# Kernel tuning notes

Measured on AMD Instinct MI355X. Metric: run time of the kernel, lower is better.

## Reference

```python
import jax, jax.numpy as jnp
import numpy as np

N_NODES = 50000
N_EDGES = 800000
IN_DIM, HIDDEN, Z_DIM = 32, 64, 32


def gcn_conv(x, W, b, src, dst, n):
    """PyG-style GCNConv: h = D^{-1/2}(A+I)D^{-1/2} (x W) + b."""
    h = x @ W  # [N, out]
    loop = jnp.arange(n, dtype=src.dtype)
    s = jnp.concatenate([src, loop])  # add self-loops
    d = jnp.concatenate([dst, loop])
    deg = jax.ops.segment_sum(jnp.ones(s.shape, h.dtype), d, num_segments=n)
    dinv = jax.lax.rsqrt(jnp.maximum(deg, jnp.asarray(1.0, h.dtype)))
    norm = dinv[s] * dinv[d]                       # [E+N]
    msg = h[s] * norm[:, None]                     # gather + scale
    out = jax.ops.segment_sum(msg, d, num_segments=n)  # scatter-add
    return out + b


def setup_inputs() -> dict:
    key = jax.random.key(0)
    ks = jax.random.split(key, 8)
    sc = lambda fan_in: 1.0 / np.sqrt(fan_in)
    x = jax.random.normal(ks[0], (N_NODES, IN_DIM), jnp.float32)
    edge_index = jax.random.randint(ks[1], (2, N_EDGES), 0, N_NODES, jnp.int64)
    W1 = jax.random.normal(ks[2], (IN_DIM, HIDDEN), jnp.float32) * sc(IN_DIM)
    b1 = jnp.zeros((HIDDEN,), jnp.float32)
    W2 = jax.random.normal(ks[3], (HIDDEN, HIDDEN), jnp.float32) * sc(HIDDEN)
    b2 = jnp.zeros((HIDDEN,), jnp.float32)
    W_mu = jax.random.normal(ks[4], (HIDDEN, Z_DIM), jnp.float32) * sc(HIDDEN)
    b_mu = jnp.zeros((Z_DIM,), jnp.float32)
    W_lv = jax.random.normal(ks[5], (HIDDEN, Z_DIM), jnp.float32) * sc(HIDDEN)
    b_lv = jnp.zeros((Z_DIM,), jnp.float32)
    eps = jax.random.normal(ks[6], (N_NODES, Z_DIM), jnp.float32)
    return {"x": x, "edge_index": edge_index, "W1": W1, "b1": b1, "W2": W2,
            "b2": b2, "W_mu": W_mu, "b_mu": b_mu, "W_lv": W_lv, "b_lv": b_lv,
            "eps": eps}


def reference(x, edge_index, W1, b1, W2, b2, W_mu, b_mu, W_lv, b_lv, eps):
    src, dst = edge_index[0], edge_index[1]
    n = x.shape[0]
    h = jax.nn.relu(gcn_conv(x, W1, b1, src, dst, n))
    h = jax.nn.relu(gcn_conv(h, W2, b2, src, dst, n))
    # dropout p=0.0 -> identity
    mu = gcn_conv(h, W_mu, b_mu, src, dst, n)
    logvar = gcn_conv(h, W_lv, b_lv, src, dst, n)
    z = mu + jnp.exp(0.5 * logvar) * eps  # reparametrize
    return (z, mu, logvar)
```

## Files before the change

### kernel.cpp

```cpp
#include <hip/hip_runtime.h>
#include <math.h>

#define N_NODES 50000
#define N_EDGES 800000
#define IN_DIM 32
#define HIDDEN 64
#define Z_DIM 32
#define SCAN_B 256
#define NB_SCAN ((N_NODES + SCAN_B - 1) / SCAN_B)
#define N_XCD 8
#define NPX ((N_NODES + N_XCD - 1) / N_XCD)
#define SLICE 2048
#define N_SLICE ((N_EDGES + SLICE - 1) / SLICE)
#define SCAT_B (N_SLICE * N_XCD)
#define FB 2048

__device__ __forceinline__ float bf2f(unsigned short u) {
    return __uint_as_float(((unsigned int)u) << 16);
}
__device__ __forceinline__ unsigned short f2bf(float f) {
    unsigned int u = __float_as_uint(f);
    u += 0x7fffu + ((u >> 16) & 1u);
    return (unsigned short)(u >> 16);
}

__device__ __forceinline__ int detect64(const int* raw) {
    int lane = threadIdx.x & 63;
    int odd = raw[2 * lane + 1];
    unsigned long long b = __ballot(odd != 0);
    return (b == 0ULL) ? 1 : 0;
}

__global__ void prep_kernel(const float* __restrict__ x, unsigned short* __restrict__ xb,
                            const void* __restrict__ raw, int* __restrict__ flag,
                            int* __restrict__ cnt, int2* __restrict__ ep0,
                            int* __restrict__ rank) {
    int is64 = detect64((const int*)raw);
    int i = blockIdx.x * 256 + threadIdx.x;
    if (blockIdx.x == 0 && threadIdx.x == 0) *flag = is64;
    if (i < N_NODES * IN_DIM) xb[i] = f2bf(x[i]);
    if (blockIdx.x < SCAT_B) {
        int xcd = blockIdx.x % N_XCD;
        int sl  = blockIdx.x / N_XCD;
        int own = ((sl % N_XCD) == xcd) ? 1 : 0;
        int lo  = xcd * NPX, hi = lo + NPX;
        int base = sl * SLICE;
#pragma unroll
        for (int j = 0; j < SLICE / 256; j++) {
            int e = base + j * 256 + threadIdx.x;
            if (e < N_EDGES) {
                int d = is64 ? (int)((const long long*)raw)[N_EDGES + e]
                             : ((const int*)raw)[N_EDGES + e];
                if (own) {
                    int s = is64 ? (int)((const long long*)raw)[e]
                                 : ((const int*)raw)[e];
                    ep0[e] = make_int2(s, d);
                }
                if (d >= lo && d < hi) rank[e] = atomicAdd(&cnt[d], 1);
            }
        }
    }
}

__global__ void scan1_kernel(const int* __restrict__ cnt, int* __restrict__ pre,
                             int* __restrict__ bsum, float* __restrict__ dinv) {
    __shared__ int s[SCAN_B];
    int t = threadIdx.x;
    int g = blockIdx.x * SCAN_B + t;
    int v = (g < N_NODES) ? cnt[g] : 0;
    if (g < N_NODES) dinv[g] = rsqrtf((float)(v + 1));
    s[t] = v;
    __syncthreads();
    for (int o = 1; o < SCAN_B; o <<= 1) {
        int add = (t >= o) ? s[t - o] : 0;
        __syncthreads();
        s[t] += add;
        __syncthreads();
    }
    if (g < N_NODES) pre[g] = s[t] - v;
    if (t == SCAN_B - 1) bsum[blockIdx.x] = s[t];
}

__global__ void scan23_kernel(int* __restrict__ rowptr, const int* __restrict__ bsum) {
    __shared__ int s[256];
    int t = threadIdx.x;
    int v = (t < NB_SCAN) ? bsum[t] : 0;
    s[t] = v;
    __syncthreads();
    for (int o = 1; o < 256; o <<= 1) {
        int add = (t >= o) ? s[t - o] : 0;
        __syncthreads();
        s[t] += add;
        __syncthreads();
    }
    int excl = s[blockIdx.x] - bsum[blockIdx.x];
    int g = blockIdx.x * SCAN_B + t;
    if (g < N_NODES) rowptr[g] += excl;
    if (g == 0) rowptr[N_NODES] = N_EDGES;
}

__global__ __launch_bounds__(256) void scatter_kernel(
        const int2* __restrict__ ep0, const int* __restrict__ rank,
        const int* __restrict__ rowptr, const float* __restrict__ dinv,
        int2* __restrict__ ep) {
    int base = blockIdx.x * SLICE;
#pragma unroll
    for (int j = 0; j < SLICE / 256; j++) {
        int e = base + j * 256 + threadIdx.x;
        if (e < N_EDGES) {
            int2 sd = ep0[e];
            int p = rowptr[sd.y] + rank[e];
            ep[p] = make_int2(sd.x, __float_as_int(dinv[sd.x]));
        }
    }
}

__device__ __forceinline__ void agg_body64(int e0, int e1, int2 pr,
                                           const int2* __restrict__ ep,
                                           const uint2* __restrict__ g2,
                                           int lane, float acc[4]) {
    int gsel = lane >> 4;
    int c    = lane & 15;
    for (int base = e0; base < e1; base += 64) {
        int cnt = e1 - base; cnt = cnt > 64 ? 64 : cnt;
        for (int j = 0; j < cnt; j += 16) {
            uint2 fv[4]; float wv[4];
#pragma unroll
            for (int u = 0; u < 4; u++) {
                int idx = j + u * 4 + gsel;
                int cl  = idx < cnt ? idx : cnt - 1;
                int s   = __builtin_amdgcn_ds_bpermute(cl << 2, pr.x);
                int w   = __builtin_amdgcn_ds_bpermute(cl << 2, pr.y);
                wv[u]   = idx < cnt ? __int_as_float(w) : 0.0f;
                fv[u]   = g2[(size_t)s * 16 + c];
            }
#pragma unroll
            for (int u = 0; u < 4; u++) {
                acc[0] = fmaf(wv[u], __uint_as_float(fv[u].x << 16),         acc[0]);
                acc[1] = fmaf(wv[u], __uint_as_float(fv[u].x & 0xffff0000u), acc[1]);
                acc[2] = fmaf(wv[u], __uint_as_float(fv[u].y << 16),         acc[2]);
                acc[3] = fmaf(wv[u], __uint_as_float(fv[u].y & 0xffff0000u), acc[3]);
            }
        }
        int nb = base + 64;
        if (nb < e1) {
            int idx = nb + lane;
            pr = ep[idx < N_EDGES ? idx : (N_EDGES - 1)];
        }
    }
}

__device__ __forceinline__ void agg_body32(int e0, int e1, int2 pr,
                                           const int2* __restrict__ ep,
                                           const uint2* __restrict__ x2,
                                           int lane, float acc[4]) {
    int gsel = lane >> 3;
    int c    = lane & 7;
    for (int base = e0; base < e1; base += 64) {
        int cnt = e1 - base; cnt = cnt > 64 ? 64 : cnt;
        for (int j = 0; j < cnt; j += 16) {
            uint2 fv[2]; float wv[2];
#pragma unroll
            for (int u = 0; u < 2; u++) {
                int idx = j + u * 8 + gsel;
                int cl  = idx < cnt ? idx : cnt - 1;
                int s   = __builtin_amdgcn_ds_bpermute(cl << 2, pr.x);
                int w   = __builtin_amdgcn_ds_bpermute(cl << 2, pr.y);
                wv[u]   = idx < cnt ? __int_as_float(w) : 0.0f;
                fv[u]   = x2[(size_t)s * 8 + c];
            }
#pragma unroll
            for (int u = 0; u < 2; u++) {
                acc[0] = fmaf(wv[u], __uint_as_float(fv[u].x << 16),         acc[0]);
                acc[1] = fmaf(wv[u], __uint_as_float(fv[u].x & 0xffff0000u), acc[1]);
                acc[2] = fmaf(wv[u], __uint_as_float(fv[u].y << 16),         acc[2]);
                acc[3] = fmaf(wv[u], __uint_as_float(fv[u].y & 0xffff0000u), acc[3]);
            }
        }
        int nb = base + 64;
        if (nb < e1) {
            int idx = nb + lane;
            pr = ep[idx < N_EDGES ? idx : (N_EDGES - 1)];
        }
    }
}

__global__ __launch_bounds__(256, 4) void fused_layer32_kernel(
        const int* __restrict__ rowptr, const int2* __restrict__ ep,
        const float* __restrict__ dinv, const unsigned short* __restrict__ xb,
        const float* __restrict__ W1, const float* __restrict__ b1,
        unsigned short* __restrict__ out) {
    __shared__ float sq[4 * 32];
    int lane = threadIdx.x & 63;
    int wav  = threadIdx.x >> 6;
    int gsel = lane >> 3;
    int c    = lane & 7;
    const uint2* x2 = (const uint2*)xb;
    float wcol[IN_DIM];
#pragma unroll
    for (int k = 0; k < IN_DIM; k++) wcol[k] = W1[k * 64 + lane];
    float bb = b1[lane];
    int wid = __builtin_amdgcn_readfirstlane((int)((blockIdx.x * blockDim.x + threadIdx.x) >> 6));
    int nw  = (gridDim.x * blockDim.x) >> 6;
    int v = wid;
    if (v >= N_NODES) return;
    int e0 = rowptr[v], e1 = rowptr[v + 1];
    float dv = dinv[v];
    uint2 hv = x2[(size_t)v * 8 + c];
    int i0 = e0 + lane;
    int2 pr = ep[i0 < N_EDGES ? i0 : (N_EDGES - 1)];
    while (v < N_NODES) {
        int vn = v + nw;
        int e0n = 0, e1n = 0;
        float dvn = 0.0f;
        uint2 hvn = make_uint2(0, 0);
        int2 prn = make_int2(0, 0);
        if (vn < N_NODES) {
            e0n = rowptr[vn]; e1n = rowptr[vn + 1];
            dvn = dinv[vn];
            hvn = x2[(size_t)vn * 8 + c];
            int in0 = e0n + lane;
            prn = ep[in0 < N_EDGES ? in0 : (N_EDGES - 1)];
        }
        float sv = (gsel == 0) ? dv : 0.0f;
        float acc[4];
        acc[0] = sv * __uint_as_float(hv.x << 16);
        acc[1] = sv * __uint_as_float(hv.x & 0xffff0000u);
        acc[2] = sv * __uint_as_float(hv.y << 16);
        acc[3] = sv * __uint_as_float(hv.y & 0xffff0000u);
        agg_body32(e0, e1, pr, ep, x2, lane, acc);
#pragma unroll
        for (int i = 0; i < 4; i++) {
            acc[i] += __shfl_xor(acc[i], 8);
            acc[i] += __shfl_xor(acc[i], 16);
            acc[i] += __shfl_xor(acc[i], 32);
        }
        if (lane < 8)
            ((float4*)(sq + wav * 32))[c] =
                make_float4(dv * acc[0], dv * acc[1], dv * acc[2], dv * acc[3]);
        float o = bb;
        const float4* q4 = (const float4*)(sq + wav * 32);
#pragma unroll
        for (int k = 0; k < IN_DIM / 4; k++) {
            float4 t = q4[k];
            o = fmaf(t.x, wcol[4 * k + 0], o);
            o = fmaf(t.y, wcol[4 * k + 1], o);
            o = fmaf(t.z, wcol[4 * k + 2], o);
            o = fmaf(t.w, wcol[4 * k + 3], o);
        }
        out[(size_t)v * 64 + lane] = f2bf(fmaxf(o, 0.0f));
        v = vn; e0 = e0n; e1 = e1n; dv = dvn; hv = hvn; pr = prn;
    }
}

__global__ __launch_bounds__(256, 4) void fused_layer64_kernel(
        const int* __restrict__ rowptr, const int2* __restrict__ ep,
        const float* __restrict__ dinv, const unsigned short* __restrict__ g,
        const float* __restrict__ W, const float* __restrict__ bias,
        unsigned short* __restrict__ out) {
    __shared__ float sq[4 * 64];
    int lane = threadIdx.x & 63;
    int wav  = threadIdx.x >> 6;
    int gsel = lane >> 4;
    int c    = lane & 15;
    const uint2* g2 = (const uint2*)g;
    float wcol[HIDDEN];
#pragma unroll
    for (int k = 0; k < HIDDEN; k++) wcol[k] = W[k * 64 + lane];
    float bb = bias[lane];
    int wid = __builtin_amdgcn_readfirstlane((int)((blockIdx.x * blockDim.x + threadIdx.x) >> 6));
    int nw  = (gridDim.x * blockDim.x) >> 6;
    int v = wid;
    if (v >= N_NODES) return;
    int e0 = rowptr[v], e1 = rowptr[v + 1];
    float dv = dinv[v];
    uint2 hv = g2[(size_t)v * 16 + c];
    int i0 = e0 + lane;
    int2 pr = ep[i0 < N_EDGES ? i0 : (N_EDGES - 1)];
    while (v < N_NODES) {
        int vn = v + nw;
        int e0n = 0, e1n = 0;
        float dvn = 0.0f;
        uint2 hvn = make_uint2(0, 0);
        int2 prn = make_int2(0, 0);
        if (vn < N_NODES) {
            e0n = rowptr[vn]; e1n = rowptr[vn + 1];
            dvn = dinv[vn];
            hvn = g2[(size_t)vn * 16 + c];
            int in0 = e0n + lane;
            prn = ep[in0 < N_EDGES ? in0 : (N_EDGES - 1)];
        }
        float sv = (gsel == 0) ? dv : 0.0f;
        float acc[4];
        acc[0] = sv * __uint_as_float(hv.x << 16);
        acc[1] = sv * __uint_as_float(hv.x & 0xffff0000u);
        acc[2] = sv * __uint_as_float(hv.y << 16);
        acc[3] = sv * __uint_as_float(hv.y & 0xffff0000u);
        agg_body64(e0, e1, pr, ep, g2, lane, acc);
#pragma unroll
        for (int i = 0; i < 4; i++) {
            acc[i] += __shfl_xor(acc[i], 16);
            acc[i] += __shfl_xor(acc[i], 32);
        }
        if (lane < 16)
            ((float4*)(sq + wav * 64))[c] =
                make_float4(dv * acc[0], dv * acc[1], dv * acc[2], dv * acc[3]);
        float o = bb;
        const float4* q4 = (const float4*)(sq + wav * 64);
#pragma unroll
        for (int k = 0; k < HIDDEN / 4; k++) {
            float4 t = q4[k];
            o = fmaf(t.x, wcol[4 * k + 0], o);
            o = fmaf(t.y, wcol[4 * k + 1], o);
            o = fmaf(t.z, wcol[4 * k + 2], o);
            o = fmaf(t.w, wcol[4 * k + 3], o);
        }
        out[(size_t)v * 64 + lane] = f2bf(fmaxf(o, 0.0f));
        v = vn; e0 = e0n; e1 = e1n; dv = dvn; hv = hvn; pr = prn;
    }
}

__global__ __launch_bounds__(256, 4) void fused_head_kernel(
        const int* __restrict__ rowptr, const int2* __restrict__ ep,
        const float* __restrict__ dinv, const unsigned short* __restrict__ g,
        const float* __restrict__ Wmu, const float* __restrict__ Wlv,
        const float* __restrict__ bmu, const float* __restrict__ blv,
        const float* __restrict__ eps, float* __restrict__ outz) {
    __shared__ float sq[4 * 64];
    int lane = threadIdx.x & 63;
    int wav  = threadIdx.x >> 6;
    int gsel = lane >> 4;
    int c    = lane & 15;
    int f = lane & 31;
    bool hi = lane >= 32;
    const uint2* g2 = (const uint2*)g;
    float wcol[HIDDEN];
#pragma unroll
    for (int k = 0; k < HIDDEN; k++)
        wcol[k] = hi ? Wlv[k * 32 + f] : Wmu[k * 32 + f];
    float bb = hi ? blv[f] : bmu[f];
    float* z  = outz;
    float* mu = outz + (size_t)N_NODES * Z_DIM;
    float* lv = outz + 2 * (size_t)N_NODES * Z_DIM;
    int wid = __builtin_amdgcn_readfirstlane((int)((blockIdx.x * blockDim.x + threadIdx.x) >> 6));
    int nw  = (gridDim.x * blockDim.x) >> 6;
    int v = wid;
    if (v >= N_NODES) return;
    int e0 = rowptr[v], e1 = rowptr[v + 1];
    float dv = dinv[v];
    uint2 hv = g2[(size_t)v * 16 + c];
    int i0 = e0 + lane;
    int2 pr = ep[i0 < N_EDGES ? i0 : (N_EDGES - 1)];
    while (v < N_NODES) {
        int vn = v + nw;
        int e0n = 0, e1n = 0;
        float dvn = 0.0f;
        uint2 hvn = make_uint2(0, 0);
        int2 prn = make_int2(0, 0);
        if (vn < N_NODES) {
            e0n = rowptr[vn]; e1n = rowptr[vn + 1];
            dvn = dinv[vn];
            hvn = g2[(size_t)vn * 16 + c];
            int in0 = e0n + lane;
            prn = ep[in0 < N_EDGES ? in0 : (N_EDGES - 1)];
        }
        float sv = (gsel == 0) ? dv : 0.0f;
        float acc[4];
        acc[0] = sv * __uint_as_float(hv.x << 16);
        acc[1] = sv * __uint_as_float(hv.x & 0xffff0000u);
        acc[2] = sv * __uint_as_float(hv.y << 16);
        acc[3] = sv * __uint_as_float(hv.y & 0xffff0000u);
        agg_body64(e0, e1, pr, ep, g2, lane, acc);
#pragma unroll
        for (int i = 0; i < 4; i++) {
            acc[i] += __shfl_xor(acc[i], 16);
            acc[i] += __shfl_xor(acc[i], 32);
        }
        if (lane < 16)
            ((float4*)(sq + wav * 64))[c] =
                make_float4(dv * acc[0], dv * acc[1], dv * acc[2], dv * acc[3]);
        float m = bb;
        const float4* q4 = (const float4*)(sq + wav * 64);
#pragma unroll
        for (int k = 0; k < HIDDEN / 4; k++) {
            float4 t = q4[k];
            m = fmaf(t.x, wcol[4 * k + 0], m);
            m = fmaf(t.y, wcol[4 * k + 1], m);
            m = fmaf(t.z, wcol[4 * k + 2], m);
            m = fmaf(t.w, wcol[4 * k + 3], m);
        }
        float ev = eps[(size_t)v * Z_DIM + f];
        float t  = expf(0.5f * m) * ev;
        float tlo = __shfl(t, lane | 32);
        size_t o = (size_t)v * Z_DIM + f;
        if (!hi) { mu[o] = m; z[o] = m + tlo; }
        else     { lv[o] = m; }
        v = vn; e0 = e0n; e1 = e1n; dv = dvn; hv = hvn; pr = prn;
    }
}

extern "C" void kernel_launch(void* const* d_in, const int* in_sizes, int n_in,
                              void* d_out, int out_size, void* d_ws, size_t ws_size,
                              hipStream_t stream) {
    const float* x   = (const float*)d_in[0];
    const void*  ei  = d_in[1];
    const float* W1  = (const float*)d_in[2];
    const float* b1  = (const float*)d_in[3];
    const float* W2  = (const float*)d_in[4];
    const float* b2  = (const float*)d_in[5];
    const float* Wmu = (const float*)d_in[6];
    const float* bmu = (const float*)d_in[7];
    const float* Wlv = (const float*)d_in[8];
    const float* blv = (const float*)d_in[9];
    const float* eps = (const float*)d_in[10];
    float* out = (float*)d_out;
    (void)in_sizes; (void)n_in; (void)out_size; (void)ws_size;

    char* ws = (char*)d_ws;
    size_t off = 0;
    auto alloc = [&](size_t bytes) -> void* {
        void* p = ws + off;
        off += (bytes + 255) & ~(size_t)255;
        return p;
    };
    int2*           ep     = (int2*)alloc(sizeof(int2) * N_EDGES);
    int2*           ep0    = (int2*)alloc(sizeof(int2) * N_EDGES);
    int*            rank   = (int*)alloc(sizeof(int) * N_EDGES);
    int*            rowptr = (int*)alloc(sizeof(int) * (N_NODES + 1));
    int*            cnt    = (int*)alloc(sizeof(int) * N_NODES);
    float*          dinv   = (float*)alloc(sizeof(float) * N_NODES);
    int*            flag   = (int*)alloc(sizeof(int) * 64);
    int*            bsum   = (int*)alloc(sizeof(int) * 256);
    unsigned short* xb     = (unsigned short*)alloc(sizeof(short) * (size_t)N_NODES * IN_DIM);
    unsigned short* G      = (unsigned short*)alloc(sizeof(short) * (size_t)N_NODES * HIDDEN);
    unsigned short* H      = (unsigned short*)alloc(sizeof(short) * (size_t)N_NODES * HIDDEN);

    hipMemsetAsync(cnt, 0, sizeof(int) * N_NODES, stream);
    prep_kernel<<<(N_NODES * IN_DIM + 255) / 256, 256, 0, stream>>>(x, xb, ei, flag, cnt, ep0, rank);
    scan1_kernel<<<NB_SCAN, SCAN_B, 0, stream>>>(cnt, rowptr, bsum, dinv);
    scan23_kernel<<<NB_SCAN, SCAN_B, 0, stream>>>(rowptr, bsum);
    scatter_kernel<<<N_SLICE, 256, 0, stream>>>(ep0, rank, rowptr, dinv, ep);
    fused_layer32_kernel<<<FB, 256, 0, stream>>>(rowptr, ep, dinv, xb, W1, b1, H);
    fused_layer64_kernel<<<FB, 256, 0, stream>>>(rowptr, ep, dinv, H, W2, b2, G);
    fused_head_kernel<<<FB, 256, 0, stream>>>(rowptr, ep, dinv, G, Wmu, Wlv, bmu, blv, eps, out);
}
```

Measured before the change: 231.2 us.

## Split edge prep into decode and padded-counter histogram kernels with 16-bit ranks

The combined prep kernel is split in two. The first decodes edges into ep0 plus a compact int32 dst array. The second builds the per-XCD degree histogram with counters padded to 16 ints, so each counter sits in its own 64-byte line and atomic contention from false sharing drops. Ranks are stored as 16-bit values and the unused flag is removed. The aggregation kernels now skip loads past the row end rather than clamping to a valid index. The cost is an extra kernel launch, a padded counter array and memset 16 times larger (3.2 MB), and a rank overflow if any node has more than 65535 in-edges.

Result: no change. 234.1 us (+1.2%).

```diff
diff --git a/kernel.cpp b/kernel.cpp
--- a/kernel.cpp
+++ b/kernel.cpp
@@ -14,6 +14,7 @@
 #define N_SLICE ((N_EDGES + SLICE - 1) / SLICE)
 #define SCAT_B (N_SLICE * N_XCD)
 #define FB 2048
+#define CPAD 16
 
 __device__ __forceinline__ float bf2f(unsigned short u) {
     return __uint_as_float(((unsigned int)u) << 16);
@@ -31,33 +32,40 @@
     return (b == 0ULL) ? 1 : 0;
 }
 
-__global__ void prep_kernel(const float* __restrict__ x, unsigned short* __restrict__ xb,
-                            const void* __restrict__ raw, int* __restrict__ flag,
-                            int* __restrict__ cnt, int2* __restrict__ ep0,
-                            int* __restrict__ rank) {
+__global__ void prep_a_kernel(const float* __restrict__ x, unsigned short* __restrict__ xb,
+                              const void* __restrict__ raw, int2* __restrict__ ep0,
+                              int* __restrict__ dstc) {
     int is64 = detect64((const int*)raw);
     int i = blockIdx.x * 256 + threadIdx.x;
-    if (blockIdx.x == 0 && threadIdx.x == 0) *flag = is64;
     if (i < N_NODES * IN_DIM) xb[i] = f2bf(x[i]);
-    if (blockIdx.x < SCAT_B) {
-        int xcd = blockIdx.x % N_XCD;
-        int sl  = blockIdx.x / N_XCD;
-        int own = ((sl % N_XCD) == xcd) ? 1 : 0;
-        int lo  = xcd * NPX, hi = lo + NPX;
-        int base = sl * SLICE;
-#pragma unroll
-        for (int j = 0; j < SLICE / 256; j++) {
-            int e = base + j * 256 + threadIdx.x;
-            if (e < N_EDGES) {
-                int d = is64 ? (int)((const long long*)raw)[N_EDGES + e]
-                             : ((const int*)raw)[N_EDGES + e];
-                if (own) {
-                    int s = is64 ? (int)((const long long*)raw)[e]
-                                 : ((const int*)raw)[e];
-                    ep0[e] = make_int2(s, d);
-                }
-                if (d >= lo && d < hi) rank[e] = atomicAdd(&cnt[d], 1);
-            }
+    if (i < N_EDGES) {
+        int s, d;
+        if (is64) {
+            s = (int)((const long long*)raw)[i];
+            d = (int)((const long long*)raw)[N_EDGES + i];
+        } else {
+            s = ((const int*)raw)[i];
+            d = ((const int*)raw)[N_EDGES + i];
+        }
+        ep0[i] = make_int2(s, d);
+        dstc[i] = d;
+    }
+}
+
+__global__ __launch_bounds__(256) void hist_kernel(const int* __restrict__ dstc,
+                                                   int* __restrict__ cnt,
+                                                   unsigned short* __restrict__ rank) {
+    int xcd = blockIdx.x % N_XCD;
+    int sl  = blockIdx.x / N_XCD;
+    int lo  = xcd * NPX, hi = lo + NPX;
+    int base = sl * SLICE;
+#pragma unroll
+    for (int j = 0; j < SLICE / 256; j++) {
+        int e = base + j * 256 + threadIdx.x;
+        if (e < N_EDGES) {
+            int d = dstc[e];
+            if (d >= lo && d < hi)
+                rank[e] = (unsigned short)atomicAdd(&cnt[(size_t)d * CPAD], 1);
         }
     }
 }
@@ -67,7 +75,7 @@
     __shared__ int s[SCAN_B];
     int t = threadIdx.x;
     int g = blockIdx.x * SCAN_B + t;
-    int v = (g < N_NODES) ? cnt[g] : 0;
+    int v = (g < N_NODES) ? cnt[(size_t)g * CPAD] : 0;
     if (g < N_NODES) dinv[g] = rsqrtf((float)(v + 1));
     s[t] = v;
     __syncthreads();
@@ -100,7 +108,7 @@
 }
 
 __global__ __launch_bounds__(256) void scatter_kernel(
-        const int2* __restrict__ ep0, const int* __restrict__ rank,
+        const int2* __restrict__ ep0, const unsigned short* __restrict__ rank,
         const int* __restrict__ rowptr, const float* __restrict__ dinv,
         int2* __restrict__ ep) {
     int base = blockIdx.x * SLICE;
@@ -109,7 +117,7 @@
         int e = base + j * 256 + threadIdx.x;
         if (e < N_EDGES) {
             int2 sd = ep0[e];
-            int p = rowptr[sd.y] + rank[e];
+            int p = rowptr[sd.y] + (int)rank[e];
             ep[p] = make_int2(sd.x, __float_as_int(dinv[sd.x]));
         }
     }
@@ -143,10 +151,7 @@
             }
         }
         int nb = base + 64;
-        if (nb < e1) {
-            int idx = nb + lane;
-            pr = ep[idx < N_EDGES ? idx : (N_EDGES - 1)];
-        }
+        if (nb + lane < e1) pr = ep[nb + lane];
     }
 }
 
@@ -178,10 +183,7 @@
             }
         }
         int nb = base + 64;
-        if (nb < e1) {
-            int idx = nb + lane;
-            pr = ep[idx < N_EDGES ? idx : (N_EDGES - 1)];
-        }
+        if (nb + lane < e1) pr = ep[nb + lane];
     }
 }
 
@@ -207,8 +209,8 @@
     int e0 = rowptr[v], e1 = rowptr[v + 1];
     float dv = dinv[v];
     uint2 hv = x2[(size_t)v * 8 + c];
-    int i0 = e0 + lane;
-    int2 pr = ep[i0 < N_EDGES ? i0 : (N_EDGES - 1)];
+    int2 pr = make_int2(0, 0);
+    if (lane < e1 - e0) pr = ep[e0 + lane];
     while (v < N_NODES) {
         int vn = v + nw;
         int e0n = 0, e1n = 0;
@@ -219,8 +221,7 @@
             e0n = rowptr[vn]; e1n = rowptr[vn + 1];
             dvn = dinv[vn];
             hvn = x2[(size_t)vn * 8 + c];
-            int in0 = e0n + lane;
-            prn = ep[in0 < N_EDGES ? in0 : (N_EDGES - 1)];
+            if (lane < e1n - e0n) prn = ep[e0n + lane];
         }
         float sv = (gsel == 0) ? dv : 0.0f;
         float acc[4];
@@ -275,8 +276,8 @@
     int e0 = rowptr[v], e1 = rowptr[v + 1];
     float dv = dinv[v];
     uint2 hv = g2[(size_t)v * 16 + c];
-    int i0 = e0 + lane;
-    int2 pr = ep[i0 < N_EDGES ? i0 : (N_EDGES - 1)];
+    int2 pr = make_int2(0, 0);
+    if (lane < e1 - e0) pr = ep[e0 + lane];
     while (v < N_NODES) {
         int vn = v + nw;
         int e0n = 0, e1n = 0;
@@ -287,8 +288,7 @@
             e0n = rowptr[vn]; e1n = rowptr[vn + 1];
             dvn = dinv[vn];
             hvn = g2[(size_t)vn * 16 + c];
-            int in0 = e0n + lane;
-            prn = ep[in0 < N_EDGES ? in0 : (N_EDGES - 1)];
+            if (lane < e1n - e0n) prn = ep[e0n + lane];
         }
         float sv = (gsel == 0) ? dv : 0.0f;
         float acc[4];
@@ -349,8 +349,8 @@
     int e0 = rowptr[v], e1 = rowptr[v + 1];
     float dv = dinv[v];
     uint2 hv = g2[(size_t)v * 16 + c];
-    int i0 = e0 + lane;
-    int2 pr = ep[i0 < N_EDGES ? i0 : (N_EDGES - 1)];
+    int2 pr = make_int2(0, 0);
+    if (lane < e1 - e0) pr = ep[e0 + lane];
     while (v < N_NODES) {
         int vn = v + nw;
         int e0n = 0, e1n = 0;
@@ -361,8 +361,7 @@
             e0n = rowptr[vn]; e1n = rowptr[vn + 1];
             dvn = dinv[vn];
             hvn = g2[(size_t)vn * 16 + c];
-            int in0 = e0n + lane;
-            prn = ep[in0 < N_EDGES ? in0 : (N_EDGES - 1)];
+            if (lane < e1n - e0n) prn = ep[e0n + lane];
         }
         float sv = (gsel == 0) ? dv : 0.0f;
         float acc[4];
@@ -425,18 +424,19 @@
     };
     int2*           ep     = (int2*)alloc(sizeof(int2) * N_EDGES);
     int2*           ep0    = (int2*)alloc(sizeof(int2) * N_EDGES);
-    int*            rank   = (int*)alloc(sizeof(int) * N_EDGES);
+    int*            dstc   = (int*)alloc(sizeof(int) * N_EDGES);
+    unsigned short* rank   = (unsigned short*)alloc(sizeof(short) * N_EDGES);
     int*            rowptr = (int*)alloc(sizeof(int) * (N_NODES + 1));
-    int*            cnt    = (int*)alloc(sizeof(int) * N_NODES);
+    int*            cnt    = (int*)alloc(sizeof(int) * (size_t)N_NODES * CPAD);
     float*          dinv   = (float*)alloc(sizeof(float) * N_NODES);
-    int*            flag   = (int*)alloc(sizeof(int) * 64);
     int*            bsum   = (int*)alloc(sizeof(int) * 256);
     unsigned short* xb     = (unsigned short*)alloc(sizeof(short) * (size_t)N_NODES * IN_DIM);
     unsigned short* G      = (unsigned short*)alloc(sizeof(short) * (size_t)N_NODES * HIDDEN);
     unsigned short* H      = (unsigned short*)alloc(sizeof(short) * (size_t)N_NODES * HIDDEN);
 
-    hipMemsetAsync(cnt, 0, sizeof(int) * N_NODES, stream);
-    prep_kernel<<<(N_NODES * IN_DIM + 255) / 256, 256, 0, stream>>>(x, xb, ei, flag, cnt, ep0, rank);
+    hipMemsetAsync(cnt, 0, sizeof(int) * (size_t)N_NODES * CPAD, stream);
+    prep_a_kernel<<<(N_NODES * IN_DIM + 255) / 256, 256, 0, stream>>>(x, xb, ei, ep0, dstc);
+    hist_kernel<<<SCAT_B, 256, 0, stream>>>(dstc, cnt, rank);
     scan1_kernel<<<NB_SCAN, SCAN_B, 0, stream>>>(cnt, rowptr, bsum, dinv);
     scan23_kernel<<<NB_SCAN, SCAN_B, 0, stream>>>(rowptr, bsum);
     scatter_kernel<<<N_SLICE, 256, 0, stream>>>(ep0, rank, rowptr, dinv, ep);
```
